# Kernel tuning notes

Hardware: AMD Instinct MI355X
Metric: run time of the kernel (lower is better)

The kernel has to match this reference:

```python
import jax, jax.numpy as jnp
import numpy as np

RATIO = 4
NUM_UPSAMPLES = 2  # log2(RATIO)
PADDING = 11       # (23 - 1) // 2


def _make_kernel():
    cdf23 = 2.0 * np.array([0.5, 0.305334091185, 0.0, -0.072698593239, 0.0,
                            0.021809577942, 0.0, -0.005192756653, 0.0,
                            0.000807762146, 0.0, -6.0081482e-05])
    d = cdf23[::-1]
    base = np.insert(cdf23, 0, d[:-1])  # length 23, symmetric
    return jnp.asarray(base, dtype=jnp.float32)


def setup_inputs() -> dict:
    key = jax.random.key(0)
    x = jax.random.normal(key, (4, 8, 256, 256), dtype=jnp.float32)
    return {"x": x, "kernel": _make_kernel()}


def _sep_circ_conv(img, kernel):
    """Depthwise separable 23-tap conv with circular padding.
    img: (bs, c, h, w). Processes all (b,c) slices as one batched conv."""
    bs, c, h, w = img.shape
    flat = img.reshape(bs * c, 1, h, w)
    # horizontal pass
    ph = jnp.pad(flat, ((0, 0), (0, 0), (0, 0), (PADDING, PADDING)), mode="wrap")
    kh = kernel.reshape(1, 1, 1, -1)
    fh = jax.lax.conv_general_dilated(ph, kh, (1, 1), "VALID",
                                      dimension_numbers=("NCHW", "OIHW", "NCHW"))
    # vertical pass
    pv = jnp.pad(fh, ((0, 0), (0, 0), (PADDING, PADDING), (0, 0)), mode="wrap")
    kv = kernel.reshape(1, 1, -1, 1)
    fv = jax.lax.conv_general_dilated(pv, kv, (1, 1), "VALID",
                                      dimension_numbers=("NCHW", "OIHW", "NCHW"))
    return fv.reshape(bs, c, h, w)


def reference(x, kernel):
    cur = x
    for k in range(NUM_UPSAMPLES):
        bs, c, h, w = cur.shape
        up = jnp.zeros((bs, c, 2 * h, 2 * w), dtype=cur.dtype)
        off = 1 if k == 0 else 0  # first stage inserts at odd positions
        up = up.at[..., off::2, off::2].set(cur)
        cur = _sep_circ_conv(up, kernel)
    return cur
```

## Files before the change

kernel.cpp:

```cpp
#include <hip/hip_runtime.h>


#define SINS 52
#define SMS 132

__device__ inline void fma4(float4& a, float t, const float4& r) {
    a.x += t * r.x; a.y += t * r.y; a.z += t * r.z; a.w += t * r.w;
}

__global__ __launch_bounds__(256, 4) void up4_fused(
    const float* __restrict__ in, const float* __restrict__ kern,
    float* __restrict__ out) {
    __shared__ float sG[80];
    __shared__ __attribute__((aligned(16))) float sMid[48][SMS];
    __shared__ __attribute__((aligned(16))) float sIn[48][SINS];

    const int tid = threadIdx.x;
    const int tX = blockIdx.x, tY = blockIdx.y, ch = blockIdx.z;
    const int W4 = 1024;

    if (tid < 80) {
        const int s = tid - 34;
        int jlo = (s - 10) >> 1;
        int jhi = (s + 11) >> 1;
        if (jlo < -11) jlo = -11;
        if (jhi > 11) jhi = 11;
        float acc = 0.f;
        for (int j = jlo; j <= jhi; ++j)
            acc += kern[11 + s - 2 * j] * kern[11 + j];
        sG[tid] = acc;
    }

    const float* inC = in + (size_t)ch * 256 * 256;
    const int N0y = 32 * tY - 9, N0x = 32 * tX - 9;
    const int gj0 = (N0x + 1) & 255;
    if (gj0 <= 208) {
#pragma unroll
        for (int it = 0; it < 3; ++it) {
            const int idx = tid + it * 256;
            if (idx < 576) {
                const int pi = idx / 12, m = idx % 12;
                const int gi = (N0y + 1 + pi + 256) & 255;
                *(float4*)&sIn[pi][4 * m] =
                    *(const float4*)&inC[gi * 256 + gj0 + 4 * m];
            }
        }
    } else {
#pragma unroll
        for (int it = 0; it < 9; ++it) {
            const int idx = tid + it * 256;
            const int pi = idx / 48, pj = idx % 48;
            const int gi = (N0y + 1 + pi + 256) & 255;
            const int gj = (N0x + 1 + pj + 256) & 255;
            sIn[pi][pj] = inC[gi * 256 + gj];
        }
    }
    __syncthreads();

    float tapA[17], tC6[6];
#pragma unroll
    for (int k = 0; k < 17; ++k) tapA[k] = sG[1 + 4 * k];
#pragma unroll
    for (int m = 0; m < 6; ++m) tC6[m] = sG[12 + 4 * m];

#pragma unroll
    for (int it = 0; it < 2; ++it) {
        const int idx = tid + it * 256;
        if (idx < 384) {
            const int t4 = 4 * (idx & 7), row = idx >> 3;
            float win[20];
#pragma unroll
            for (int m = 0; m < 5; ++m)
                *(float4*)&win[4 * m] = *(const float4*)&sIn[row][t4 + 4 * m];
#pragma unroll
            for (int q = 0; q < 4; ++q) {
                float a0 = 0.f, a1 = 0.f, a2 = 0.f, a3 = 0.f;
#pragma unroll
                for (int k = 0; k < 17; ++k) {
                    const float w = win[q + 16 - k];
                    a1 += tapA[k] * w;
                    a3 += tapA[16 - k] * w;
                    if (k >= 3 && k <= 14) {
                        const int m2 = k - 3;
                        a0 += tC6[m2 < 6 ? m2 : 11 - m2] * w;
                    }
                    if (k == 8) a2 = w;
                }
                float4 v; v.x = a0; v.y = a1; v.z = a2; v.w = a3;
                *(float4*)&sMid[row][4 * (t4 + q)] = v;
            }
        }
    }
    __syncthreads();

    const int c = tid & 31, gp = tid >> 5;
    float4 A[4][4];
#pragma unroll
    for (int i = 0; i < 4; ++i)
#pragma unroll
        for (int p = 0; p < 4; ++p) { A[i][p].x = 0.f; A[i][p].y = 0.f; A[i][p].z = 0.f; A[i][p].w = 0.f; }

#pragma unroll
    for (int d = 1; d <= 20; ++d) {
        const float4 R = *(const float4*)&sMid[4 * gp + d - 1][4 * c];
#pragma unroll
        for (int i = 0; i < 4; ++i) {
            const int k = i + 17 - d;
            if (k < 0 || k > 16) continue;
            fma4(A[i][1], tapA[k], R);
            fma4(A[i][3], tapA[16 - k], R);
            if (k >= 3 && k <= 14) {
                const int m = k - 3;
                fma4(A[i][0], tC6[m < 6 ? m : 11 - m], R);
            }
            if (k == 8) A[i][2] = R;
        }
    }

    float* outC = out + (size_t)ch * 1024 * 1024;
    const int row0 = 128 * tY + 16 * gp, col = 128 * tX + 4 * c;
#pragma unroll
    for (int i = 0; i < 4; ++i)
#pragma unroll
        for (int p = 0; p < 4; ++p)
            *(float4*)&outC[(size_t)(row0 + 4 * i + p) * W4 + col] = A[i][p];
}

extern "C" void kernel_launch(void* const* d_in, const int* in_sizes, int n_in,
                              void* d_out, int out_size, void* d_ws, size_t ws_size,
                              hipStream_t stream) {
    const float* x    = (const float*)d_in[0];
    const float* kern = (const float*)d_in[1];
    float* out  = (float*)d_out;

    dim3 grid(8, 8, 32);
    up4_fused<<<grid, dim3(256), 0, stream>>>(x, kern, out);
}
```

Baseline: 149.3 us.

## Shrink per-thread register footprint in horizontal and vertical passes

The horizontal pass now has each thread compute one output column per row over six iterations, reading taps straight from shared memory instead of from a 20-float register window. The vertical pass drops the 16-float4 accumulator array. It handles one row group at a time and streams 17 shared loads per group. The passthrough phase (p=2) is written as a separate copy from sMid. The aim is lower register pressure and better occupancy, at the cost of more LDS reads and a reordered store pattern.

```diff
diff --git a/kernel.cpp b/kernel.cpp
--- a/kernel.cpp
+++ b/kernel.cpp
@@ -17,7 +17,6 @@
 
     const int tid = threadIdx.x;
     const int tX = blockIdx.x, tY = blockIdx.y, ch = blockIdx.z;
-    const int W4 = 1024;
 
     if (tid < 80) {
         const int s = tid - 34;
@@ -64,66 +63,60 @@
     for (int m = 0; m < 6; ++m) tC6[m] = sG[12 + 4 * m];
 
 #pragma unroll
-    for (int it = 0; it < 2; ++it) {
+    for (int it = 0; it < 6; ++it) {
         const int idx = tid + it * 256;
-        if (idx < 384) {
-            const int t4 = 4 * (idx & 7), row = idx >> 3;
-            float win[20];
+        const int c = idx & 31, row = idx >> 5;
+        float a0 = 0.f, a1 = 0.f, a2 = 0.f, a3 = 0.f;
 #pragma unroll
-            for (int m = 0; m < 5; ++m)
-                *(float4*)&win[4 * m] = *(const float4*)&sIn[row][t4 + 4 * m];
-#pragma unroll
-            for (int q = 0; q < 4; ++q) {
-                float a0 = 0.f, a1 = 0.f, a2 = 0.f, a3 = 0.f;
-#pragma unroll
-                for (int k = 0; k < 17; ++k) {
-                    const float w = win[q + 16 - k];
-                    a1 += tapA[k] * w;
-                    a3 += tapA[16 - k] * w;
-                    if (k >= 3 && k <= 14) {
-                        const int m2 = k - 3;
-                        a0 += tC6[m2 < 6 ? m2 : 11 - m2] * w;
-                    }
-                    if (k == 8) a2 = w;
-                }
-                float4 v; v.x = a0; v.y = a1; v.z = a2; v.w = a3;
-                *(float4*)&sMid[row][4 * (t4 + q)] = v;
+        for (int k = 0; k < 17; ++k) {
+            const float w = sIn[row][c + 16 - k];
+            a1 += tapA[k] * w;
+            a3 += tapA[16 - k] * w;
+            if (k >= 3 && k <= 14) {
+                const int m2 = k - 3;
+                a0 += tC6[m2 < 6 ? m2 : 11 - m2] * w;
             }
+            if (k == 8) a2 = w;
         }
+        float4 v; v.x = a0; v.y = a1; v.z = a2; v.w = a3;
+        *(float4*)&sMid[row][4 * c] = v;
     }
     __syncthreads();
 
-    const int c = tid & 31, gp = tid >> 5;
-    float4 A[4][4];
-#pragma unroll
-    for (int i = 0; i < 4; ++i)
-#pragma unroll
-        for (int p = 0; p < 4; ++p) { A[i][p].x = 0.f; A[i][p].y = 0.f; A[i][p].z = 0.f; A[i][p].w = 0.f; }
+    float* outC = out + (size_t)ch * 1024 * 1024;
+    const int orow0 = 128 * tY, ocol0 = 128 * tX;
 
 #pragma unroll
-    for (int d = 1; d <= 20; ++d) {
-        const float4 R = *(const float4*)&sMid[4 * gp + d - 1][4 * c];
+    for (int it = 0; it < 4; ++it) {
+        const int idx = tid + it * 256;
+        const int r = idx >> 5, cc = idx & 31;
+        const float4 v = *(const float4*)&sMid[r + 8][4 * cc];
+        *(float4*)&outC[(size_t)(orow0 + 4 * r + 2) * 1024 + ocol0 + 4 * cc] = v;
+    }
+
+    const int c = tid & 31, gp = tid >> 5;
 #pragma unroll
-        for (int i = 0; i < 4; ++i) {
-            const int k = i + 17 - d;
-            if (k < 0 || k > 16) continue;
-            fma4(A[i][1], tapA[k], R);
-            fma4(A[i][3], tapA[16 - k], R);
+    for (int i = 0; i < 4; ++i) {
+        const int R0 = 4 * gp + i;
+        float4 a0, a1, a3;
+        a0.x = a0.y = a0.z = a0.w = 0.f;
+        a1.x = a1.y = a1.z = a1.w = 0.f;
+        a3.x = a3.y = a3.z = a3.w = 0.f;
+#pragma unroll
+        for (int k = 0; k < 17; ++k) {
+            const float4 R = *(const float4*)&sMid[R0 + 16 - k][4 * c];
+            fma4(a1, tapA[k], R);
+            fma4(a3, tapA[16 - k], R);
             if (k >= 3 && k <= 14) {
                 const int m = k - 3;
-                fma4(A[i][0], tC6[m < 6 ? m : 11 - m], R);
+                fma4(a0, tC6[m < 6 ? m : 11 - m], R);
             }
-            if (k == 8) A[i][2] = R;
         }
+        const size_t rbase = (size_t)(orow0 + 4 * R0) * 1024 + ocol0 + 4 * c;
+        *(float4*)&outC[rbase]            = a0;
+        *(float4*)&outC[rbase + 1024]     = a1;
+        *(float4*)&outC[rbase + 3 * 1024] = a3;
     }
-
-    float* outC = out + (size_t)ch * 1024 * 1024;
-    const int row0 = 128 * tY + 16 * gp, col = 128 * tX + 4 * c;
-#pragma unroll
-    for (int i = 0; i < 4; ++i)
-#pragma unroll
-        for (int p = 0; p < 4; ++p)
-            *(float4*)&outC[(size_t)(row0 + 4 * i + p) * W4 + col] = A[i][p];
 }
 
 extern "C" void kernel_launch(void* const* d_in, const int* in_sizes, int n_in,
```

Result: slower. 213.5 us (+43.0%).
